# Optimization experiments

Measured on AMD Instinct MI355X. Metric: run time of the kernel, lower is better.

The kernel has to match this reference:

```python
import jax, jax.numpy as jnp
import numpy as np

B, T = 1, 1024
V, C, H, L = 50304, 768, 12, 6
K = C // H              # 64, d_head
F = int(C * 3.5) // 32 * 32   # 2688, d_ffn
GN_EPS = 6.4e-4


def _layernorm(x, wb, eps=1e-5):
    mu = x.mean(-1, keepdims=True)
    var = jnp.var(x, axis=-1, keepdims=True)
    return (x - mu) * jax.lax.rsqrt(var + eps) * wb[0] + wb[1]


def _groupnorm(x, wb):  # x: [N, C], groups of size K per head
    xg = x.reshape(-1, H, K)
    mu = xg.mean(-1, keepdims=True)
    var = jnp.var(xg, axis=-1, keepdims=True)
    xg = (xg - mu) * jax.lax.rsqrt(var + GN_EPS)
    return xg.reshape(-1, C) * wb[0] + wb[1]


def _lerp(a, b, w):  # torch.lerp(a, b, w) = a + (b - a) * w
    return a + (b - a) * w


def _shift(x):  # token-shift with zero initial state (fresh LayerState)
    return jnp.concatenate([jnp.zeros_like(x[:, :1]), x[:, :-1]], axis=1)


def _layer(x, p):
    (tm_ln, tm_ts, Wr, Wk, Wv, Wg, Wo, bonus, decay, tm_gn,
     cm_ln, cm_ts, Win, Wout, cWg) = p
    # ---- time mixer ----
    xn = _layernorm(x, tm_ln)
    xp = _shift(xn)
    r = (_lerp(xp, xn, tm_ts[0]) @ Wr).reshape(B, T, H, K)
    k = (_lerp(xp, xn, tm_ts[1]) @ Wk).reshape(B, T, H, K)
    v = (_lerp(xp, xn, tm_ts[2]) @ Wv).reshape(B, T, H, K)
    g = _lerp(xp, xn, tm_ts[3]) @ Wg
    w = jnp.exp(-jnp.exp(decay))  # [H, K] per-channel decay

    def wkv_step(kv, rkv):  # kv: [B,H,K,V]
        r_t, k_t, v_t = rkv  # each [B,H,K]
        a = k_t[..., :, None] * v_t[..., None, :]          # outer product kv_t
        out = jnp.einsum('bhk,bhkv->bhv', r_t, kv + a * bonus[..., None])
        return kv * w[..., None] + a, out

    kv0 = jnp.zeros((B, H, K, K), x.dtype)
    kv_final, out = jax.lax.scan(
        wkv_step, kv0,
        (r.transpose(1, 0, 2, 3), k.transpose(1, 0, 2, 3),
         v.transpose(1, 0, 2, 3)))
    out = out.transpose(1, 0, 2, 3).reshape(B, T, C)
    out = _groupnorm(out.reshape(B * T, C), tm_gn).reshape(B, T, C)
    x = x + (out * jax.nn.silu(g)) @ Wo
    # ---- channel mixer ----
    xn = _layernorm(x, cm_ln)
    xp = _shift(xn)
    h = jnp.square(jax.nn.relu(_lerp(xp, xn, cm_ts[0]) @ Win))
    x = x + (h @ Wout) * jax.nn.sigmoid(_lerp(xp, xn, cm_ts[1]) @ cWg)
    return x, kv_final


def _forward(tokens, embed, embed_ln, tm_ln, tm_ts, tm_Wr, tm_Wk, tm_Wv,
             tm_Wg, tm_Wo, tm_bonus, tm_decay, tm_gn, cm_ln, cm_ts, cm_Win,
             cm_Wout, cm_Wg, head_ln, unembed):
    x = _layernorm(embed[tokens], embed_ln)
    stacked = (tm_ln, tm_ts, tm_Wr, tm_Wk, tm_Wv, tm_Wg, tm_Wo, tm_bonus,
               tm_decay, tm_gn, cm_ln, cm_ts, cm_Win, cm_Wout, cm_Wg)
    x, _ = jax.lax.scan(_layer, x, stacked)  # scan over the L layers
    return _layernorm(x, head_ln) @ unembed  # logits [B, T, V]


def setup_inputs() -> dict:
    key = jax.random.key(0)
    ks = iter(jax.random.split(key, 48))

    def rn(shape, s=0.02):
        return s * jax.random.normal(next(ks), shape, jnp.float32)

    def ln(pre=()):  # stacked (weight, bias) of a LayerNorm/GroupNorm
        return jnp.stack([1.0 + rn(pre + (C,)), rn(pre + (C,))], axis=len(pre))

    return {
        'tokens': jax.random.randint(next(ks), (B, T), 0, V),
        'embed': rn((V, C)),
        'embed_ln': ln(),
        'tm_ln': ln((L,)),
        'tm_ts': jax.random.uniform(next(ks), (L, 4, C), jnp.float32),
        'tm_Wr': rn((L, C, C)),
        'tm_Wk': rn((L, C, C)),
        'tm_Wv': rn((L, C, C)),
        'tm_Wg': rn((L, C, C)),
        'tm_Wo': rn((L, C, C)),
        'tm_bonus': rn((L, H, K), 0.5),
        'tm_decay': rn((L, H, K), 0.5),
        'tm_gn': ln((L,)),
        'cm_ln': ln((L,)),
        'cm_ts': jax.random.uniform(next(ks), (L, 2, C), jnp.float32),
        'cm_Win': rn((L, C, F)),
        'cm_Wout': rn((L, F, C)),
        'cm_Wg': rn((L, C, C)),
        'head_ln': ln(),
        'unembed': rn((C, V)),
    }


def reference(tokens, embed, embed_ln, tm_ln, tm_ts, tm_Wr, tm_Wk, tm_Wv,
              tm_Wg, tm_Wo, tm_bonus, tm_decay, tm_gn, cm_ln, cm_ts, cm_Win,
              cm_Wout, cm_Wg, head_ln, unembed):
    return _forward(tokens, embed, embed_ln, tm_ln, tm_ts, tm_Wr, tm_Wk,
                    tm_Wv, tm_Wg, tm_Wo, tm_bonus, tm_decay, tm_gn, cm_ln,
                    cm_ts, cm_Win, cm_Wout, cm_Wg, head_ln, unembed)
```

## Files before the change

kernel.cpp:

```cpp
#include <hip/hip_runtime.h>
#include <hip/hip_bf16.h>

#define T_LEN 1024
#define CDIM  768
#define HNUM  12
#define KDIM  64
#define LNUM  6
#define FDIM  2688
#define VDIM  50304
#define NCH   16
#define LCH   64

#define WSZ   (CDIM * CDIM)
#define WIN_OFF  (6 * WSZ)
#define WOUT_OFF (WIN_OFF + CDIM * FDIM)
#define WBUF_ELEMS (WOUT_OFF + FDIM * CDIM)

typedef __attribute__((ext_vector_type(4))) float f32x4;
typedef __attribute__((ext_vector_type(8))) short s16x8;

__device__ __forceinline__ ushort f2bf(float f) {
    union { float fv; unsigned u; } v; v.fv = f;
    unsigned r = v.u + 0x7fffu + ((v.u >> 16) & 1u);
    return (ushort)(r >> 16);
}

__device__ __forceinline__ void gload_lds16(const ushort* g, ushort* l) {
    __builtin_amdgcn_global_load_lds(
        (const __attribute__((address_space(1))) void*)g,
        (__attribute__((address_space(3))) void*)l, 16, 0, 0);
}

template <int N_>
__device__ __forceinline__ void wait_vm() {
    if constexpr (N_ == 0)       asm volatile("s_waitcnt vmcnt(0)" ::: "memory");
    else if constexpr (N_ == 6)  asm volatile("s_waitcnt vmcnt(6)" ::: "memory");
    else if constexpr (N_ == 8)  asm volatile("s_waitcnt vmcnt(8)" ::: "memory");
    else if constexpr (N_ == 12) asm volatile("s_waitcnt vmcnt(12)" ::: "memory");
    else                         asm volatile("s_waitcnt vmcnt(16)" ::: "memory");
}
__device__ __forceinline__ void barrier_asm() {
    asm volatile("s_barrier" ::: "memory");
}

__device__ __forceinline__ size_t frag_idx(int nn, int k, int K) {
    int n16 = nn >> 4, ln15 = nn & 15;
    int k64 = k >> 6, s = (k >> 5) & 1, kq = (k >> 3) & 3;
    return ((size_t)(n16 * (K >> 6) + k64) * 2 + s) * 512 + (kq * 16 + ln15) * 8
           + (k & 4);
}

__device__ __forceinline__ void trans_quad_reg(const float* __restrict__ in,
        ushort* __restrict__ out, int R, int C, int tkq, int tnp) {
    int tid = threadIdx.x;
    int k4 = tid >> 4, n4 = tid & 15;
    int kb = (tkq << 7) + k4 * 4;
    int nb = (tnp << 7) + n4 * 4;
    float4 v[2][2][4];
    #pragma unroll
    for (int dk = 0; dk < 2; dk++)
        #pragma unroll
        for (int dn = 0; dn < 2; dn++)
            #pragma unroll
            for (int j = 0; j < 4; j++)
                v[dk][dn][j] = *(const float4*)
                    &in[(size_t)(kb + dk * 64 + j) * C + nb + dn * 64];
    #pragma unroll
    for (int dk = 0; dk < 2; dk++)
        #pragma unroll
        for (int dn = 0; dn < 2; dn++) {
            const float* f0 = (const float*)&v[dk][dn][0];
            const float* f1 = (const float*)&v[dk][dn][1];
            const float* f2 = (const float*)&v[dk][dn][2];
            const float* f3 = (const float*)&v[dk][dn][3];
            #pragma unroll
            for (int e = 0; e < 4; e++) {
                ushort4 u;
                u.x = f2bf(f0[e]); u.y = f2bf(f1[e]);
                u.z = f2bf(f2[e]); u.w = f2bf(f3[e]);
                *(ushort4*)&out[frag_idx(nb + dn * 64 + e, kb + dk * 64, R)] = u;
            }
        }
}

__device__ __forceinline__ void trans_tile(const float* __restrict__ in,
        ushort* __restrict__ out, int R, int C, int tk, int tn) {
    __shared__ float tile[64][65];
    int tid = threadIdx.x;
    int r = tid >> 4, c4 = (tid & 15) << 2;
    int k0 = tk << 6, n0 = tn << 6;
    #pragma unroll
    for (int j = 0; j < 4; j++) {
        int rr = r + j * 16;
        float4 f = *(const float4*)&in[(size_t)(k0 + rr) * C + n0 + c4];
        tile[rr][c4 + 0] = f.x; tile[rr][c4 + 1] = f.y;
        tile[rr][c4 + 2] = f.z; tile[rr][c4 + 3] = f.w;
    }
    __syncthreads();
    #pragma unroll
    for (int j = 0; j < 4; j++) {
        int n = r + j * 16;
        ushort4 u;
        u.x = f2bf(tile[c4 + 0][n]);
        u.y = f2bf(tile[c4 + 1][n]);
        u.z = f2bf(tile[c4 + 2][n]);
        u.w = f2bf(tile[c4 + 3][n]);
        *(ushort4*)&out[frag_idx(n0 + n, k0 + c4, R)] = u;
    }
}

__global__ __launch_bounds__(256)
void k_trans(const float* __restrict__ in, ushort* __restrict__ out, int R, int C) {
    trans_tile(in, out, R, C, blockIdx.y, blockIdx.x);
}

__device__ __forceinline__ void embed_ln_row(int t, const int* __restrict__ tok,
        const float* __restrict__ embed, const float* __restrict__ wb,
        float* __restrict__ xout) {
    int tid = threadIdx.x;
    const float* row = embed + (size_t)tok[t] * CDIM;
    float v[3]; float s = 0.f, s2 = 0.f;
    #pragma unroll
    for (int j = 0; j < 3; j++) {
        v[j] = row[tid + j * 256]; s += v[j]; s2 += v[j] * v[j];
    }
    #pragma unroll
    for (int m = 32; m; m >>= 1) { s += __shfl_xor(s, m); s2 += __shfl_xor(s2, m); }
    __shared__ float rs[4], rq[4];
    int w = tid >> 6;
    if ((tid & 63) == 0) { rs[w] = s; rq[w] = s2; }
    __syncthreads();
    s = rs[0] + rs[1] + rs[2] + rs[3];
    s2 = rq[0] + rq[1] + rq[2] + rq[3];
    float mu = s * (1.f / CDIM);
    float inv = rsqrtf(s2 * (1.f / CDIM) - mu * mu + 1e-5f);
    #pragma unroll
    for (int j = 0; j < 3; j++) {
        int c = tid + j * 256;
        xout[(size_t)t * CDIM + c] = (v[j] - mu) * inv * wb[c] + wb[CDIM + c];
    }
}

__global__ __launch_bounds__(256)
void k_embed_ln(const int* __restrict__ tok, const float* __restrict__ embed,
                const float* __restrict__ wb, float* __restrict__ xout) {
    embed_ln_row(blockIdx.x, tok, embed, wb, xout);
}

__device__ __forceinline__ void conv_layer_quad(int t,
        const float* p0, const float* p1, const float* p2, const float* p3,
        const float* p4, const float* p5, const float* pWin, const float* pWout,
        ushort* wl) {
    const float* in; ushort* out; int R, C, tkq, tnp;
    if (t < 216) {
        int mi = t / 36, tt = t % 36;
        switch (mi) {
            case 0: in = p0; break; case 1: in = p1; break;
            case 2: in = p2; break; case 3: in = p3; break;
            case 4: in = p4; break; default: in = p5; break;
        }
        out = wl + (size_t)mi * WSZ; R = 768; C = 768;
        tkq = tt / 6; tnp = tt % 6;
    } else if (t < 342) {
        int tt = t - 216;
        in = pWin; out = wl + WIN_OFF; R = 768; C = 2688;
        tkq = tt / 21; tnp = tt % 21;
    } else {
        int tt = t - 342;
        in = pWout; out = wl + WOUT_OFF; R = 2688; C = 768;
        tkq = tt / 6; tnp = tt % 6;
    }
    trans_quad_reg(in, out, R, C, tkq, tnp);
}

__global__ __launch_bounds__(256)
void k_conv_layer(const float* p0, const float* p1, const float* p2,
                  const float* p3, const float* p4, const float* p5,
                  const float* pWin, const float* pWout, ushort* wl) {
    int t = blockIdx.x;
    const float* in; ushort* out; int R, C, tk, tn;
    if (t < 864) {
        int mi = t / 144, tt = t % 144;
        switch (mi) {
            case 0: in = p0; break; case 1: in = p1; break;
            case 2: in = p2; break; case 3: in = p3; break;
            case 4: in = p4; break; default: in = p5; break;
        }
        out = wl + (size_t)mi * WSZ; R = 768; C = 768;
        tk = tt / 12; tn = tt % 12;
    } else if (t < 1368) {
        int tt = t - 864;
        in = pWin; out = wl + WIN_OFF; R = 768; C = 2688;
        tk = tt / 42; tn = tt % 42;
    } else {
        int tt = t - 1368;
        in = pWout; out = wl + WOUT_OFF; R = 2688; C = 768;
        tk = tt / 12; tn = tt % 12;
    }
    trans_tile(in, out, R, C, tk, tn);
}

__global__ __launch_bounds__(256)
void k_conv_all(const float* Wr, const float* Wk, const float* Wv,
                const float* Wg, const float* Wo, const float* Wcg,
                const float* Win, const float* Wout, const float* unemb,
                ushort* wbuf, ushort* ubuf,
                const int* tok, const float* embed, const float* eln, float* x) {
    int b = blockIdx.x;
    if (b < 6 * 468) {
        int l = b / 468, t = b % 468;
        conv_layer_quad(t,
            Wr + (size_t)l * WSZ, Wk + (size_t)l * WSZ, Wv + (size_t)l * WSZ,
            Wg + (size_t)l * WSZ, Wo + (size_t)l * WSZ, Wcg + (size_t)l * WSZ,
            Win + (size_t)l * CDIM * FDIM, Wout + (size_t)l * FDIM * CDIM,
            wbuf + (size_t)l * WBUF_ELEMS);
    } else if (b < 6 * 468 + 2358) {
        int t = b - 6 * 468;
        int tkq = t / 393, tnp = t % 393;
        trans_quad_reg(unemb, ubuf, CDIM, VDIM, tkq, tnp);
    } else {
        embed_ln_row(b - (6 * 468 + 2358), tok, embed, eln, x);
    }
}

__global__ __launch_bounds__(256)
void k_ln_bf(const float* __restrict__ x, const float* __restrict__ wb,
             ushort* __restrict__ out) {
    int t = blockIdx.x, tid = threadIdx.x;
    float v[3]; float s = 0.f, s2 = 0.f;
    #pragma unroll
    for (int j = 0; j < 3; j++) {
        v[j] = x[(size_t)t * CDIM + tid + j * 256];
        s += v[j]; s2 += v[j] * v[j];
    }
    #pragma unroll
    for (int m = 32; m; m >>= 1) { s += __shfl_xor(s, m); s2 += __shfl_xor(s2, m); }
    __shared__ float rs[4], rq[4];
    int w = tid >> 6;
    if ((tid & 63) == 0) { rs[w] = s; rq[w] = s2; }
    __syncthreads();
    s = rs[0] + rs[1] + rs[2] + rs[3];
    s2 = rq[0] + rq[1] + rq[2] + rq[3];
    float mu = s * (1.f / CDIM);
    float inv = rsqrtf(s2 * (1.f / CDIM) - mu * mu + 1e-5f);
    #pragma unroll
    for (int j = 0; j < 3; j++) {
        int c = tid + j * 256;
        out[(size_t)t * CDIM + c] = f2bf((v[j] - mu) * inv * wb[c] + wb[CDIM + c]);
    }
}

template <int NM>
__global__ __launch_bounds__(256)
void k_lnlerp(const float* __restrict__ x, const float* __restrict__ lnw,
              const float* __restrict__ ts, ushort* __restrict__ mix) {
    int t = blockIdx.x, tid = threadIdx.x;
    bool has = (t > 0);
    float vb[3], va[3];
    float sb = 0.f, qb = 0.f, sa = 0.f, qa = 0.f;
    #pragma unroll
    for (int j = 0; j < 3; j++) {
        int c = tid + j * 256;
        vb[j] = x[(size_t)t * CDIM + c];
        sb += vb[j]; qb += vb[j] * vb[j];
        va[j] = has ? x[(size_t)(t - 1) * CDIM + c] : 0.f;
        sa += va[j]; qa += va[j] * va[j];
    }
    #pragma unroll
    for (int m = 32; m; m >>= 1) {
        sb += __shfl_xor(sb, m); qb += __shfl_xor(qb, m);
        sa += __shfl_xor(sa, m); qa += __shfl_xor(qa, m);
    }
    __shared__ float r0[4], r1[4], r2[4], r3[4];
    int w = tid >> 6;
    if ((tid & 63) == 0) { r0[w] = sb; r1[w] = qb; r2[w] = sa; r3[w] = qa; }
    __syncthreads();
    sb = r0[0] + r0[1] + r0[2] + r0[3]; qb = r1[0] + r1[1] + r1[2] + r1[3];
    sa = r2[0] + r2[1] + r2[2] + r2[3]; qa = r3[0] + r3[1] + r3[2] + r3[3];
    float mub = sb * (1.f / CDIM);
    float invb = rsqrtf(qb * (1.f / CDIM) - mub * mub + 1e-5f);
    float mua = sa * (1.f / CDIM);
    float inva = rsqrtf(qa * (1.f / CDIM) - mua * mua + 1e-5f);
    #pragma unroll
    for (int j = 0; j < 3; j++) {
        int c = tid + j * 256;
        float wgt = lnw[c], bia = lnw[CDIM + c];
        float xb = (vb[j] - mub) * invb * wgt + bia;
        float xa = has ? (va[j] - mua) * inva * wgt + bia : 0.f;
        #pragma unroll
        for (int m = 0; m < NM; m++) {
            float tv = ts[m * CDIM + c];
            mix[((size_t)m * T_LEN + t) * CDIM + c] = f2bf(xa + (xb - xa) * tv);
        }
    }
}

template <int BM, int BN, int EPI>
__device__ __forceinline__ void gemm_body(
        const ushort* __restrict__ A, const ushort* __restrict__ Bf,
        float* __restrict__ Cf, ushort* __restrict__ Cb,
        const float* __restrict__ resid, const float* __restrict__ gate,
        int N, int K, int mb, int nb, ushort* Al) {
    const int tid = threadIdx.x, lane = tid & 63, wave = tid >> 6;
    constexpr int WM = BM / 2, WN = BN / 2, FM = WM / 16, FN = WN / 16;
    const int wm = (wave >> 1) * WM, wn = (wave & 1) * WN;
    constexpr int AR = BM / 32;
    constexpr int LD = AR + 2 * FN;
    const int kq = lane >> 4, ln15 = lane & 15;

    const size_t bstride = (size_t)(K >> 6) * 2048;
    const char* bbase = (const char*)Bf +
        (size_t)((nb + wn) >> 4) * bstride + lane * 16;

    auto stageA = [&](int buf, int kt) {
        int k0 = kt << 6;
        #pragma unroll
        for (int r = 0; r < AR; r++) {
            int slot = tid + r * 256;
            int row = slot >> 3, g = slot & 7;
            int gk = ((g ^ (row & 7)) << 3);
            gload_lds16(A + (size_t)(mb + row) * K + k0 + gk,
                        &Al[buf * BM * 64 + slot * 8]);
        }
    };
    auto loadB = [&](s16x8 (&dst)[2][FN], int kt) {
        const char* p = bbase + (size_t)kt * 2048;
        #pragma unroll
        for (int s = 0; s < 2; s++)
            #pragma unroll
            for (int j = 0; j < FN; j++)
                dst[s][j] = *(const s16x8*)(p + (size_t)j * bstride + s * 1024);
    };

    f32x4 acc[FM][FN];
    #pragma unroll
    for (int i = 0; i < FM; i++)
        #pragma unroll
        for (int j = 0; j < FN; j++) acc[i][j] = (f32x4)0.f;

    auto compute = [&](const ushort* Ab, s16x8 (&bfr)[2][FN]) {
        #pragma unroll
        for (int s = 0; s < 2; s++) {
            s16x8 af[FM];
            #pragma unroll
            for (int i = 0; i < FM; i++) {
                int row = wm + i * 16 + ln15;
                int g = (s * 4 + kq) ^ (row & 7);
                af[i] = *(const s16x8*)&Ab[row * 64 + g * 8];
            }
            #pragma unroll
            for (int i = 0; i < FM; i++)
                #pragma unroll
                for (int j = 0; j < FN; j++)
                    acc[i][j] = __builtin_amdgcn_mfma_f32_16x16x32_bf16(
                        af[i], bfr[s][j], acc[i][j], 0, 0, 0);
        }
    };

    const int nt = K >> 6;
    s16x8 b0[2][FN], b1[2][FN];
    stageA(0, 0); loadB(b0, 0);
    stageA(1, 1); loadB(b1, 1);
    for (int t = 0; t < nt; t += 2) {
        wait_vm<LD>();
        barrier_asm();
        compute(Al, b0);
        barrier_asm();
        if (t + 2 < nt) { stageA(0, t + 2); loadB(b0, t + 2); }
        if (t + 2 < nt) wait_vm<LD>();
        else            wait_vm<0>();
        barrier_asm();
        compute(Al + BM * 64, b1);
        barrier_asm();
        if (t + 3 < nt) { stageA(1, t + 3); loadB(b1, t + 3); }
    }
    #pragma unroll
    for (int i = 0; i < FM; i++) {
        int rbase = mb + wm + i * 16 + (lane >> 4) * 4;
        #pragma unroll
        for (int j = 0; j < FN; j++) {
            int col = nb + wn + j * 16 + (lane & 15);
            #pragma unroll
            for (int r = 0; r < 4; r++) {
                size_t idx = (size_t)(rbase + r) * N + col;
                float vv = acc[i][j][r];
                if constexpr (EPI == 0) {
                    Cf[idx] = vv;
                } else if constexpr (EPI == 1) {
                    Cf[idx] = resid[idx] + vv;
                } else if constexpr (EPI == 2) {
                    float z = vv > 0.f ? vv * vv : 0.f;
                    Cb[idx] = f2bf(z);
                } else {
                    float gv = gate[idx];
                    Cf[idx] = resid[idx] + vv / (1.f + __expf(-gv));
                }
            }
        }
    }
}

template <int BM, int BN, int EPI, bool BATCH>
__global__ __launch_bounds__(256)
void k_gemm_std(const ushort* __restrict__ A, const ushort* __restrict__ Bf,
                float* __restrict__ Cf, ushort* __restrict__ Cb,
                const float* __restrict__ resid, const float* __restrict__ gate,
                int N, int K) {
    __shared__ __align__(16) ushort Al[2 * BM * 64];
    if constexpr (BATCH) {
        int z = blockIdx.z;
        A  += (size_t)z * T_LEN * CDIM;
        Bf += (size_t)z * CDIM * CDIM;
        Cf += (size_t)z * T_LEN * CDIM;
    }
    gemm_body<BM, BN, EPI>(A, Bf, Cf, Cb, resid, gate, N, K,
                           blockIdx.y * BM, blockIdx.x * BN, Al);
}

__global__ __launch_bounds__(256)
void k_gemm_head(const ushort* __restrict__ A, const ushort* __restrict__ Bf,
                 float* __restrict__ C) {
    __shared__ __align__(16) ushort Al[2 * 128 * 64];
    __shared__ __align__(16) ushort Bl[2 * 128 * 64];
    int id = blockIdx.x;
    int xcd = id & 7, slot = id >> 3;
    int mbi = slot & 7, nbl = slot >> 3;
    int nbi = nbl * 8 + xcd;
    if (nbi >= VDIM / 128) return;
    const int mb = mbi * 128, nb = nbi * 128;
    const int tid = threadIdx.x, lane = tid & 63, wave = tid >> 6;
    const int wm = (wave >> 1) * 64, wn = (wave & 1) * 64;
    const int kq = lane >> 4, ln15 = lane & 15;
    constexpr int K = CDIM, N = VDIM;
    const size_t bstride = (size_t)(K >> 6) * 1024;

    auto stage = [&](int buf, int kt) {
        int k0 = kt << 6;
        #pragma unroll
        for (int r = 0; r < 4; r++) {
            int slot2 = tid + r * 256;
            int row = slot2 >> 3, g = slot2 & 7;
            int gk = ((g ^ (row & 7)) << 3);
            gload_lds16(A + (size_t)(mb + row) * K + k0 + gk,
                        &Al[buf * 8192 + slot2 * 8]);
        }
        #pragma unroll
        for (int r = 0; r < 4; r++) {
            int slot2 = tid + r * 256;
            int n16 = slot2 >> 7, off = slot2 & 127;
            gload_lds16(Bf + (size_t)((nb >> 4) + n16) * bstride
                           + (size_t)kt * 1024 + off * 8,
                        &Bl[buf * 8192 + slot2 * 8]);
        }
    };

    f32x4 acc[4][4];
    #pragma unroll
    for (int i = 0; i < 4; i++)
        #pragma unroll
        for (int j = 0; j < 4; j++) acc[i][j] = (f32x4)0.f;

    stage(0, 0);
    stage(1, 1);
    for (int t = 0; t < 12; t++) {
        if (t < 11) wait_vm<8>();
        else        wait_vm<0>();
        barrier_asm();
        const ushort* Ab = &Al[(t & 1) * 8192];
        #pragma unroll
        for (int s = 0; s < 2; s++) {
            s16x8 af[4], bfr[4];
            #pragma unroll
            for (int i = 0; i < 4; i++) {
                int row = wm + i * 16 + ln15;
                int g = (s * 4 + kq) ^ (row & 7);
                af[i] = *(const s16x8*)&Ab[row * 64 + g * 8];
            }
            #pragma unroll
            for (int j = 0; j < 4; j++) {
                int n16 = (wn >> 4) + j;
                bfr[j] = *(const s16x8*)&Bl[(t & 1) * 8192 + n16 * 1024
                                            + (s * 512) + lane * 8];
            }
            #pragma unroll
            for (int i = 0; i < 4; i++)
                #pragma unroll
                for (int j = 0; j < 4; j++)
                    acc[i][j] = __builtin_amdgcn_mfma_f32_16x16x32_bf16(
                        af[i], bfr[j], acc[i][j], 0, 0, 0);
        }
        barrier_asm();
        if (t + 2 < 12) stage(t & 1, t + 2);
    }
    #pragma unroll
    for (int i = 0; i < 4; i++) {
        int rbase = mb + wm + i * 16 + (lane >> 4) * 4;
        #pragma unroll
        for (int j = 0; j < 4; j++) {
            int col = nb + wn + j * 16 + ln15;
            #pragma unroll
            for (int r = 0; r < 4; r++)
                C[(size_t)(rbase + r) * N + col] = acc[i][j][r];
        }
    }
}

__global__ __launch_bounds__(256)
void k_cmix(const ushort* __restrict__ mix, const ushort* __restrict__ wl,
            ushort* __restrict__ hb, float* __restrict__ gcm) {
    __shared__ __align__(16) ushort Al[2 * 128 * 64];
    int bx = blockIdx.x, mb = blockIdx.y * 128;
    if (bx < FDIM / 64) {
        gemm_body<128, 64, 2>(mix, wl + WIN_OFF, nullptr, hb, nullptr, nullptr,
                              FDIM, CDIM, mb, bx * 64, Al);
    } else {
        gemm_body<128, 64, 0>(mix + (size_t)T_LEN * CDIM, wl + 5 * WSZ, gcm,
                              nullptr, nullptr, nullptr, CDIM, CDIM, mb,
                              (bx - FDIM / 64) * 64, Al);
    }
}

__global__ __launch_bounds__(256)
void k_wkv1(const float* __restrict__ kb, const float* __restrict__ vb,
            const float* __restrict__ decay, float* __restrict__ Stil) {
    int c = blockIdx.x / HNUM, h = blockIdx.x % HNUM;
    __shared__ float kl[4096], vl[4096], wsh[64];
    int tid = threadIdx.x;
    for (int idx = tid; idx < 4096; idx += 256) {
        int j = idx >> 6, cc = idx & 63;
        size_t g = (size_t)(c * LCH + j) * CDIM + h * 64 + cc;
        kl[idx] = kb[g]; vl[idx] = vb[g];
    }
    if (tid < 64) wsh[tid] = expf(-expf(decay[h * 64 + tid]));
    __syncthreads();
    int k = tid >> 2, v0 = (tid & 3) * 16;
    float w = wsh[k], f = 1.f;
    float s[16];
    #pragma unroll
    for (int i = 0; i < 16; i++) s[i] = 0.f;
    for (int j = 63; j >= 0; --j) {
        float kw = kl[j * 64 + k] * f;
        #pragma unroll
        for (int i = 0; i < 16; i++) s[i] += kw * vl[j * 64 + v0 + i];
        f *= w;
    }
    float* dst = Stil + ((size_t)(c * HNUM + h) << 12) + k * 64 + v0;
    #pragma unroll
    for (int i = 0; i < 16; i++) dst[i] = s[i];
}

__global__ __launch_bounds__(256)
void k_wkv23(const float* __restrict__ rb, const float* __restrict__ kb,
             const float* __restrict__ vb, const float* __restrict__ Stil,
             const float* __restrict__ decay, const float* __restrict__ bonus,
             const float* __restrict__ gate, const float* __restrict__ gnw,
             ushort* __restrict__ y) {
    int c = blockIdx.x / HNUM, h = blockIdx.x % HNUM;
    __shared__ float rl[4096], kl[4096], vl[4096];
    __shared__ float part[4][4096];
    __shared__ float wsh[64], bsh[64];
    int tid = threadIdx.x;
    for (int idx = tid; idx < 4096; idx += 256) {
        int j = idx >> 6, cc = idx & 63;
        size_t g = (size_t)(c * LCH + j) * CDIM + h * 64 + cc;
        rl[idx] = rb[g]; kl[idx] = kb[g]; vl[idx] = vb[g];
    }
    if (tid < 64) {
        wsh[tid] = expf(-expf(decay[h * 64 + tid]));
        bsh[tid] = bonus[h * 64 + tid];
    }
    __syncthreads();
    int v = tid & 63, kg = tid >> 6;
    float S[16], wr[16], br[16], w64[16];
    #pragma unroll
    for (int i = 0; i < 16; i++) {
        S[i] = 0.f;
        wr[i] = wsh[kg * 16 + i];
        br[i] = bsh[kg * 16 + i];
        float t2 = wr[i];
        t2 *= t2; t2 *= t2; t2 *= t2; t2 *= t2; t2 *= t2; t2 *= t2;
        w64[i] = t2;
    }
    for (int cc = 0; cc < c; cc++) {
        const float* sp = Stil + ((size_t)(cc * HNUM + h) << 12);
        #pragma unroll
        for (int i = 0; i < 16; i++)
            S[i] = S[i] * w64[i] + sp[(kg * 16 + i) * 64 + v];
    }
    for (int j = 0; j < 64; j++) {
        float vj = vl[j * 64 + v];
        const float4* kp = (const float4*)&kl[j * 64 + kg * 16];
        const float4* rp = (const float4*)&rl[j * 64 + kg * 16];
        float rsum = 0.f;
        #pragma unroll
        for (int qq = 0; qq < 4; qq++) {
            float4 k4 = kp[qq], r4 = rp[qq];
            const float* kf = (const float*)&k4;
            const float* rf = (const float*)&r4;
            #pragma unroll
            for (int e = 0; e < 4; e++) {
                int i = qq * 4 + e;
                float a = kf[e] * vj;
                rsum += rf[e] * (S[i] + a * br[i]);
                S[i] = S[i] * wr[i] + a;
            }
        }
        part[kg][j * 64 + v] = rsum;
    }
    __syncthreads();
    for (int jj = 0; jj < 16; jj++) {
        int j = kg * 16 + jj;
        float o = part[0][j * 64 + v] + part[1][j * 64 + v] +
                  part[2][j * 64 + v] + part[3][j * 64 + v];
        float s = o, s2 = o * o;
        #pragma unroll
        for (int m = 32; m; m >>= 1) { s += __shfl_xor(s, m); s2 += __shfl_xor(s2, m); }
        float mu = s * (1.f / 64.f);
        float var = s2 * (1.f / 64.f) - mu * mu;
        float xg = (o - mu) * rsqrtf(var + 6.4e-4f);
        int t = c * LCH + j, col = h * 64 + v;
        float gv = gate[(size_t)t * CDIM + col];
        float silu = gv / (1.f + __expf(-gv));
        y[(size_t)t * CDIM + col] = f2bf((xg * gnw[col] + gnw[CDIM + col]) * silu);
    }
}

extern "C" void kernel_launch(void* const* d_in, const int* in_sizes, int n_in,
                              void* d_out, int out_size, void* d_ws, size_t ws_size,
                              hipStream_t stream) {
    const int*   tok      = (const int*)d_in[0];
    const float* embed    = (const float*)d_in[1];
    const float* embed_ln = (const float*)d_in[2];
    const float* tm_ln    = (const float*)d_in[3];
    const float* tm_ts    = (const float*)d_in[4];
    const float* tm_Wr    = (const float*)d_in[5];
    const float* tm_Wk    = (const float*)d_in[6];
    const float* tm_Wv    = (const float*)d_in[7];
    const float* tm_Wg    = (const float*)d_in[8];
    const float* tm_Wo    = (const float*)d_in[9];
    const float* tm_bonus = (const float*)d_in[10];
    const float* tm_decay = (const float*)d_in[11];
    const float* tm_gn    = (const float*)d_in[12];
    const float* cm_ln    = (const float*)d_in[13];
    const float* cm_ts    = (const float*)d_in[14];
    const float* cm_Win   = (const float*)d_in[15];
    const float* cm_Wout  = (const float*)d_in[16];
    const float* cm_Wg    = (const float*)d_in[17];
    const float* head_ln  = (const float*)d_in[18];
    const float* unembed  = (const float*)d_in[19];
    float* out = (float*)d_out;

    const size_t TC = (size_t)T_LEN * CDIM;
    char* wp = (char*)d_ws;
    auto alloc = [&](size_t bytes) {
        char* p = wp; wp += (bytes + 255) & ~(size_t)255; return p;
    };
    float*  x    = (float*)alloc(TC * 4);
    ushort* mix  = (ushort*)alloc(4 * TC * 2);
    float*  rkvg = (float*)alloc(4 * TC * 4);
    float*  gcm  = (float*)alloc(TC * 4);
    ushort* y    = (ushort*)alloc(TC * 2);
    ushort* hb   = (ushort*)alloc((size_t)T_LEN * FDIM * 2);
    float*  Stil = (float*)alloc((size_t)NCH * HNUM * 4096 * 4);
    ushort* ubuf = (ushort*)alloc((size_t)CDIM * VDIM * 2);
    size_t fixed_bytes = (size_t)(wp - (char*)d_ws);
    const size_t per_layer = ((size_t)WBUF_ELEMS * 2 + 255) & ~(size_t)255;
    bool all6 = (fixed_bytes + 6 * per_layer) <= ws_size;
    ushort* wbuf = (ushort*)alloc(all6 ? 6 * per_layer : per_layer);
    if ((size_t)(wp - (char*)d_ws) > ws_size) return;

    if (all6) {
        k_conv_all<<<6 * 468 + 2358 + 1024, 256, 0, stream>>>(
            tm_Wr, tm_Wk, tm_Wv, tm_Wg, tm_Wo, cm_Wg, cm_Win, cm_Wout,
            unembed, wbuf, ubuf, tok, embed, embed_ln, x);
    } else {
        k_trans<<<dim3(VDIM / 64, CDIM / 64), 256, 0, stream>>>(
            unembed, ubuf, CDIM, VDIM);
        k_embed_ln<<<T_LEN, 256, 0, stream>>>(tok, embed, embed_ln, x);
    }

    dim3 g64(CDIM / 64, T_LEN / 64);
    dim3 gQKVG(CDIM / 64, T_LEN / 128, 4);
    dim3 gCmix(FDIM / 64 + CDIM / 64, T_LEN / 128);

    for (int l = 0; l < LNUM; l++) {
        ushort* wl = all6 ? (ushort*)((char*)wbuf + (size_t)l * per_layer) : wbuf;
        if (!all6) {
            const size_t lo = (size_t)l * CDIM * CDIM;
            k_conv_layer<<<1872, 256, 0, stream>>>(
                tm_Wr + lo, tm_Wk + lo, tm_Wv + lo, tm_Wg + lo, tm_Wo + lo,
                cm_Wg + lo, cm_Win + (size_t)l * CDIM * FDIM,
                cm_Wout + (size_t)l * FDIM * CDIM, wl);
        }
        const float* dec = tm_decay + (size_t)l * HNUM * KDIM;
        const float* bon = tm_bonus + (size_t)l * HNUM * KDIM;

        k_lnlerp<4><<<T_LEN, 256, 0, stream>>>(x, tm_ln + (size_t)l * 2 * CDIM,
                                               tm_ts + (size_t)l * 4 * CDIM, mix);
        k_gemm_std<128,64,0,true><<<gQKVG, 256, 0, stream>>>(
            mix, wl, rkvg, nullptr, nullptr, nullptr, CDIM, CDIM);
        k_wkv1<<<NCH * HNUM, 256, 0, stream>>>(rkvg + TC, rkvg + 2 * TC, dec, Stil);
        k_wkv23<<<NCH * HNUM, 256, 0, stream>>>(rkvg, rkvg + TC, rkvg + 2 * TC,
            Stil, dec, bon, rkvg + 3 * TC, tm_gn + (size_t)l * 2 * CDIM, y);
        k_gemm_std<64,64,1,false><<<g64, 256, 0, stream>>>(
            y, wl + 4 * WSZ, x, nullptr, x, nullptr, CDIM, CDIM);

        k_lnlerp<2><<<T_LEN, 256, 0, stream>>>(x, cm_ln + (size_t)l * 2 * CDIM,
                                               cm_ts + (size_t)l * 2 * CDIM, mix);
        k_cmix<<<gCmix, 256, 0, stream>>>(mix, wl, hb, gcm);
        k_gemm_std<64,64,3,false><<<g64, 256, 0, stream>>>(
            hb, wl + WOUT_OFF, x, nullptr, x, gcm, CDIM, FDIM);
    }

    k_ln_bf<<<T_LEN, 256, 0, stream>>>(x, head_ln, mix);
    k_gemm_head<<<3200, 256, 0, stream>>>(mix, ubuf, out);
}
```

Baseline: 882.8 us.

## Replace LDS-staged GEMM with register-direct A/B loads and smaller tiles

The shared GEMM body no longer stages A tiles into LDS with global_load_lds and barriers. Each wave now loads its A and B MFMA fragments straight from global memory into registers, double-buffered. The QKVG and channel-mix GEMMs also drop from 128-row to 64-row tiles, which doubles the number of blocks. This removes LDS traffic and barrier syncs and adds parallelism, at the cost of redundant global A reads across waves that share rows, and less coalesced strided A loads.

```diff
diff --git a/kernel.cpp b/kernel.cpp
--- a/kernel.cpp
+++ b/kernel.cpp
@@ -34,9 +34,7 @@
 template <int N_>
 __device__ __forceinline__ void wait_vm() {
     if constexpr (N_ == 0)       asm volatile("s_waitcnt vmcnt(0)" ::: "memory");
-    else if constexpr (N_ == 6)  asm volatile("s_waitcnt vmcnt(6)" ::: "memory");
     else if constexpr (N_ == 8)  asm volatile("s_waitcnt vmcnt(8)" ::: "memory");
-    else if constexpr (N_ == 12) asm volatile("s_waitcnt vmcnt(12)" ::: "memory");
     else                         asm volatile("s_waitcnt vmcnt(16)" ::: "memory");
 }
 __device__ __forceinline__ void barrier_asm() {
@@ -296,40 +294,34 @@
 }
 
 template <int BM, int BN, int EPI>
-__device__ __forceinline__ void gemm_body(
+__device__ __forceinline__ void gemm_reg(
         const ushort* __restrict__ A, const ushort* __restrict__ Bf,
         float* __restrict__ Cf, ushort* __restrict__ Cb,
         const float* __restrict__ resid, const float* __restrict__ gate,
-        int N, int K, int mb, int nb, ushort* Al) {
+        int N, int K, int mb, int nb) {
     const int tid = threadIdx.x, lane = tid & 63, wave = tid >> 6;
     constexpr int WM = BM / 2, WN = BN / 2, FM = WM / 16, FN = WN / 16;
     const int wm = (wave >> 1) * WM, wn = (wave & 1) * WN;
-    constexpr int AR = BM / 32;
-    constexpr int LD = AR + 2 * FN;
     const int kq = lane >> 4, ln15 = lane & 15;
-
-    const size_t bstride = (size_t)(K >> 6) * 2048;
-    const char* bbase = (const char*)Bf +
-        (size_t)((nb + wn) >> 4) * bstride + lane * 16;
-
-    auto stageA = [&](int buf, int kt) {
-        int k0 = kt << 6;
-        #pragma unroll
-        for (int r = 0; r < AR; r++) {
-            int slot = tid + r * 256;
-            int row = slot >> 3, g = slot & 7;
-            int gk = ((g ^ (row & 7)) << 3);
-            gload_lds16(A + (size_t)(mb + row) * K + k0 + gk,
-                        &Al[buf * BM * 64 + slot * 8]);
-        }
+    const size_t bstride = (size_t)(K >> 6) * 1024;
+    const ushort* abase = A + (size_t)(mb + wm + ln15) * K + kq * 8;
+    const ushort* bbase = Bf + (size_t)((nb + wn) >> 4) * bstride + lane * 8;
+
+    auto loadA = [&](s16x8 (&a)[2][FM], int kt) {
+        #pragma unroll
+        for (int s = 0; s < 2; s++)
+            #pragma unroll
+            for (int i = 0; i < FM; i++)
+                a[s][i] = *(const s16x8*)(abase + (size_t)(i * 16) * K
+                                          + kt * 64 + s * 32);
     };
-    auto loadB = [&](s16x8 (&dst)[2][FN], int kt) {
-        const char* p = bbase + (size_t)kt * 2048;
+    auto loadB = [&](s16x8 (&b)[2][FN], int kt) {
         #pragma unroll
         for (int s = 0; s < 2; s++)
             #pragma unroll
             for (int j = 0; j < FN; j++)
-                dst[s][j] = *(const s16x8*)(p + (size_t)j * bstride + s * 1024);
+                b[s][j] = *(const s16x8*)(bbase + (size_t)j * bstride
+                                          + (size_t)kt * 1024 + s * 512);
     };
 
     f32x4 acc[FM][FN];
@@ -338,48 +330,33 @@
         #pragma unroll
         for (int j = 0; j < FN; j++) acc[i][j] = (f32x4)0.f;
 
-    auto compute = [&](const ushort* Ab, s16x8 (&bfr)[2][FN]) {
-        #pragma unroll
-        for (int s = 0; s < 2; s++) {
-            s16x8 af[FM];
-            #pragma unroll
-            for (int i = 0; i < FM; i++) {
-                int row = wm + i * 16 + ln15;
-                int g = (s * 4 + kq) ^ (row & 7);
-                af[i] = *(const s16x8*)&Ab[row * 64 + g * 8];
-            }
+    auto comp = [&](s16x8 (&a)[2][FM], s16x8 (&b)[2][FN]) {
+        #pragma unroll
+        for (int s = 0; s < 2; s++)
             #pragma unroll
             for (int i = 0; i < FM; i++)
                 #pragma unroll
                 for (int j = 0; j < FN; j++)
                     acc[i][j] = __builtin_amdgcn_mfma_f32_16x16x32_bf16(
-                        af[i], bfr[s][j], acc[i][j], 0, 0, 0);
-        }
+                        a[s][i], b[s][j], acc[i][j], 0, 0, 0);
     };
 
     const int nt = K >> 6;
-    s16x8 b0[2][FN], b1[2][FN];
-    stageA(0, 0); loadB(b0, 0);
-    stageA(1, 1); loadB(b1, 1);
+    s16x8 a0[2][FM], a1[2][FM], b0[2][FN], b1[2][FN];
+    loadA(a0, 0); loadB(b0, 0);
+    loadA(a1, 1); loadB(b1, 1);
     for (int t = 0; t < nt; t += 2) {
-        wait_vm<LD>();
-        barrier_asm();
-        compute(Al, b0);
-        barrier_asm();
-        if (t + 2 < nt) { stageA(0, t + 2); loadB(b0, t + 2); }
-        if (t + 2 < nt) wait_vm<LD>();
-        else            wait_vm<0>();
-        barrier_asm();
-        compute(Al + BM * 64, b1);
-        barrier_asm();
-        if (t + 3 < nt) { stageA(1, t + 3); loadB(b1, t + 3); }
+        comp(a0, b0);
+        if (t + 2 < nt) { loadA(a0, t + 2); loadB(b0, t + 2); }
+        comp(a1, b1);
+        if (t + 3 < nt) { loadA(a1, t + 3); loadB(b1, t + 3); }
     }
     #pragma unroll
     for (int i = 0; i < FM; i++) {
         int rbase = mb + wm + i * 16 + (lane >> 4) * 4;
         #pragma unroll
         for (int j = 0; j < FN; j++) {
-            int col = nb + wn + j * 16 + (lane & 15);
+            int col = nb + wn + j * 16 + ln15;
             #pragma unroll
             for (int r = 0; r < 4; r++) {
                 size_t idx = (size_t)(rbase + r) * N + col;
@@ -406,15 +383,28 @@
                 float* __restrict__ Cf, ushort* __restrict__ Cb,
                 const float* __restrict__ resid, const float* __restrict__ gate,
                 int N, int K) {
-    __shared__ __align__(16) ushort Al[2 * BM * 64];
     if constexpr (BATCH) {
         int z = blockIdx.z;
         A  += (size_t)z * T_LEN * CDIM;
         Bf += (size_t)z * CDIM * CDIM;
         Cf += (size_t)z * T_LEN * CDIM;
     }
-    gemm_body<BM, BN, EPI>(A, Bf, Cf, Cb, resid, gate, N, K,
-                           blockIdx.y * BM, blockIdx.x * BN, Al);
+    gemm_reg<BM, BN, EPI>(A, Bf, Cf, Cb, resid, gate, N, K,
+                          blockIdx.y * BM, blockIdx.x * BN);
+}
+
+__global__ __launch_bounds__(256)
+void k_cmix(const ushort* __restrict__ mix, const ushort* __restrict__ wl,
+            ushort* __restrict__ hb, float* __restrict__ gcm) {
+    int bx = blockIdx.x, mb = blockIdx.y * 64;
+    if (bx < FDIM / 64) {
+        gemm_reg<64, 64, 2>(mix, wl + WIN_OFF, nullptr, hb, nullptr, nullptr,
+                            FDIM, CDIM, mb, bx * 64);
+    } else {
+        gemm_reg<64, 64, 0>(mix + (size_t)T_LEN * CDIM, wl + 5 * WSZ, gcm,
+                            nullptr, nullptr, nullptr, CDIM, CDIM, mb,
+                            (bx - FDIM / 64) * 64);
+    }
 }
 
 __global__ __launch_bounds__(256)
@@ -502,21 +492,6 @@
             for (int r = 0; r < 4; r++)
                 C[(size_t)(rbase + r) * N + col] = acc[i][j][r];
         }
-    }
-}
-
-__global__ __launch_bounds__(256)
-void k_cmix(const ushort* __restrict__ mix, const ushort* __restrict__ wl,
-            ushort* __restrict__ hb, float* __restrict__ gcm) {
-    __shared__ __align__(16) ushort Al[2 * 128 * 64];
-    int bx = blockIdx.x, mb = blockIdx.y * 128;
-    if (bx < FDIM / 64) {
-        gemm_body<128, 64, 2>(mix, wl + WIN_OFF, nullptr, hb, nullptr, nullptr,
-                              FDIM, CDIM, mb, bx * 64, Al);
-    } else {
-        gemm_body<128, 64, 0>(mix + (size_t)T_LEN * CDIM, wl + 5 * WSZ, gcm,
-                              nullptr, nullptr, nullptr, CDIM, CDIM, mb,
-                              (bx - FDIM / 64) * 64, Al);
     }
 }
 
@@ -680,8 +655,8 @@
     }
 
     dim3 g64(CDIM / 64, T_LEN / 64);
-    dim3 gQKVG(CDIM / 64, T_LEN / 128, 4);
-    dim3 gCmix(FDIM / 64 + CDIM / 64, T_LEN / 128);
+    dim3 gQKVG(CDIM / 64, T_LEN / 64, 4);
+    dim3 gCmix(FDIM / 64 + CDIM / 64, T_LEN / 64);
 
     for (int l = 0; l < LNUM; l++) {
         ushort* wl = all6 ? (ushort*)((char*)wbuf + (size_t)l * per_layer) : wbuf;
@@ -697,7 +672,7 @@
 
         k_lnlerp<4><<<T_LEN, 256, 0, stream>>>(x, tm_ln + (size_t)l * 2 * CDIM,
                                                tm_ts + (size_t)l * 4 * CDIM, mix);
-        k_gemm_std<128,64,0,true><<<gQKVG, 256, 0, stream>>>(
+        k_gemm_std<64,64,0,true><<<gQKVG, 256, 0, stream>>>(
             mix, wl, rkvg, nullptr, nullptr, nullptr, CDIM, CDIM);
         k_wkv1<<<NCH * HNUM, 256, 0, stream>>>(rkvg + TC, rkvg + 2 * TC, dec, Stil);
         k_wkv23<<<NCH * HNUM, 256, 0, stream>>>(rkvg, rkvg + TC, rkvg + 2 * TC,
```

Result: slower. 1.049 ms (+18.8%).
